# Kernel optimization log

Hardware: AMD Instinct MI355X
Metric: run time of the kernel (lower is better)

## Reference

```python
import jax, jax.numpy as jnp
import numpy as np


def _elu(x):
    return jnp.where(x > 0, x, jnp.expm1(x))


def setup_inputs() -> dict:
    key = jax.random.key(0)
    ks = jax.random.split(key, 12)
    B, T, E, A, S, H, L = 1024, 50, 1024, 6, 200, 200, 30
    g = lambda k, shape, s=0.05: (jax.random.normal(k, shape, jnp.float32) * s)
    return {
        "action": jax.random.normal(ks[0], (B, T, A), jnp.float32),
        "embed": jax.random.normal(ks[1], (B, T, E), jnp.float32),
        "noise": jax.random.normal(ks[2], (B, T, L), jnp.float32),
        # GRUCell params (PyTorch gate order r,z,n), stored as [in, 3S]
        "W_ih": g(ks[3], (A + E, 3 * S)),
        "W_hh": g(ks[4], (S, 3 * S)),
        "b_ih": jnp.zeros((3 * S,), jnp.float32),
        "b_hh": jnp.zeros((3 * S,), jnp.float32),
        # fc_prior: Linear(S,H) -> ELU -> Linear(H, 2L)
        "Wp1": g(ks[5], (S, H)), "bp1": jnp.zeros((H,), jnp.float32),
        "Wp2": g(ks[6], (H, 2 * L)), "bp2": jnp.zeros((2 * L,), jnp.float32),
        # fc_posterior: Linear(S+E,H) -> ELU -> Linear(H, 2L)
        "Wq1": g(ks[7], (S + E, H)), "bq1": jnp.zeros((H,), jnp.float32),
        "Wq2": g(ks[8], (H, 2 * L)), "bq2": jnp.zeros((2 * L,), jnp.float32),
    }


def reference(action, embed, noise, W_ih, W_hh, b_ih, b_hh,
              Wp1, bp1, Wp2, bp2, Wq1, bq1, Wq2, bq2):
    B = action.shape[0]
    S = W_hh.shape[0]

    def gru(x, h):
        # PyTorch GRUCell: gates r, z, n
        gi = x @ W_ih + b_ih
        gh = h @ W_hh + b_hh
        i_r, i_z, i_n = jnp.split(gi, 3, -1)
        h_r, h_z, h_n = jnp.split(gh, 3, -1)
        r = jax.nn.sigmoid(i_r + h_r)
        z = jax.nn.sigmoid(i_z + h_z)
        n = jnp.tanh(i_n + r * h_n)
        return (1.0 - z) * n + z * h

    def step(deter, inp):
        a_t, e_t, eps_t = inp  # [B,A], [B,E], [B,L]
        deter = gru(jnp.concatenate([a_t, e_t], -1), deter)
        pm, ps = jnp.split(_elu(deter @ Wp1 + bp1) @ Wp2 + bp2, 2, -1)
        qm, qs = jnp.split(
            _elu(jnp.concatenate([deter, e_t], -1) @ Wq1 + bq1) @ Wq2 + bq2, 2, -1)
        ps = jax.nn.softplus(ps) + 0.1
        qs = jax.nn.softplus(qs) + 0.1
        stoch = qm + qs * eps_t  # posterior rsample
        return deter, (deter, stoch, pm, ps, qm, qs)

    deter0 = jnp.zeros((B, S), action.dtype)
    xs = (jnp.swapaxes(action, 0, 1),
          jnp.swapaxes(embed, 0, 1),
          jnp.swapaxes(noise, 0, 1))
    _, outs = jax.lax.scan(step, deter0, xs)
    # [T,B,*] -> [B,T,*]; pack (deter, stoch, prior mean/std, post mean/std)
    outs = [jnp.swapaxes(o, 0, 1) for o in outs]
    return jnp.concatenate(outs, -1)  # [B, T, S + 5L]
```

## Files before the change

### kernel.cpp

```cpp
#include <hip/hip_runtime.h>
#include <hip/hip_bf16.h>
#include <cstdint>


typedef __attribute__((ext_vector_type(8))) short   short8;
typedef __attribute__((ext_vector_type(8))) __bf16  bf16x8;
typedef __attribute__((ext_vector_type(4))) float   f32x4;

__device__ __forceinline__ float bf2f(unsigned short u) {
    unsigned int v = ((unsigned int)u) << 16;
    return __builtin_bit_cast(float, v);
}
__device__ __forceinline__ unsigned short f2bf(float f) {
    unsigned int v = __builtin_bit_cast(unsigned int, f);
    v = v + 0x7FFFu + ((v >> 16) & 1u);
    return (unsigned short)(v >> 16);
}
__device__ __forceinline__ float softplusf(float x) {
    return (x > 20.f) ? x : log1pf(__expf(x));
}
__device__ __forceinline__ void gload_lds16(const void* g, void* l) {
    __builtin_amdgcn_global_load_lds(
        (const __attribute__((address_space(1))) void*)g,
        (__attribute__((address_space(3))) void*)l, 16, 0, 0);
}

#define OFF_BPACK 81920000
#define OFF_WHH   83558400
#define OFF_WPQ1  83837952
#define OFF_WPQ2  84024320


__global__ __launch_bounds__(256) void pack_kernel(
    const float* __restrict__ W_ih, const float* __restrict__ W_hh,
    const float* __restrict__ Wp1,  const float* __restrict__ Wq1,
    const float* __restrict__ Wp2,  const float* __restrict__ Wq2,
    unsigned short* __restrict__ Bpack, unsigned short* __restrict__ Whh_p,
    unsigned short* __restrict__ Wpq1,  unsigned short* __restrict__ Wpq2)
{
    int e = blockIdx.x * 256 + threadIdx.x;
    if (e < 819200) {
        const int j = e & 7, l = (e >> 3) & 63;
        const int nt = (e >> 9) % 50, kk = e / (512 * 50);
        const int k = kk * 32 + (l >> 4) * 8 + j;
        const int c = nt * 16 + (l & 15);
        Bpack[e] = f2bf((c < 600) ? W_ih[(6 + k) * 600 + c]
                                  : Wq1[(200 + k) * 200 + (c - 600)]);
        return;
    }
    e -= 819200;
    if (e < 139776) {
        const int j = e & 7, l = (e >> 3) & 63;
        const int nt = (e >> 9) % 39, kk = e / (512 * 39);
        const int k = kk * 32 + (l >> 4) * 8 + j;
        const int g = nt / 13, st = nt % 13;
        const int c = st * 16 + (l & 15);
        Whh_p[e] = (k < 200 && c < 200) ? f2bf(W_hh[k * 600 + g * 200 + c]) : (unsigned short)0;
        return;
    }
    e -= 139776;
    if (e < 93184) {
        const int j = e & 7, l = (e >> 3) & 63;
        const int nt = (e >> 9) % 26, kk = e / (512 * 26);
        const int k = kk * 32 + (l >> 4) * 8 + j;
        unsigned short v = 0;
        if (nt < 13) { const int c = nt * 16 + (l & 15);        if (k < 200 && c < 200) v = f2bf(Wp1[k * 200 + c]); }
        else         { const int c = (nt - 13) * 16 + (l & 15); if (k < 200 && c < 200) v = f2bf(Wq1[k * 200 + c]); }
        Wpq1[e] = v;
        return;
    }
    e -= 93184;
    if (e < 28672) {
        const int j = e & 7, l = (e >> 3) & 63;
        const int nt = (e >> 9) % 8, kk = e / (512 * 8);
        const int k = kk * 32 + (l >> 4) * 8 + j;
        unsigned short v = 0;
        if (nt < 4) { const int c = nt * 16 + (l & 15);       if (k < 200 && c < 60) v = f2bf(Wp2[k * 60 + c]); }
        else        { const int c = (nt - 4) * 16 + (l & 15); if (k < 200 && c < 60) v = f2bf(Wq2[k * 60 + c]); }
        Wpq2[e] = v;
    }
}

__global__ __launch_bounds__(512, 4) void k1_gi(
    const float* __restrict__ embed,
    const float* __restrict__ action,
    const float* __restrict__ W_ih,
    const float* __restrict__ b_ih,
    const float* __restrict__ bq1,
    const unsigned short* __restrict__ Bpack,
    unsigned short* __restrict__ GI)
{
    __shared__ unsigned short Bb[2][12800];
    __shared__ unsigned short Ab[2][2048];

    const int tid = threadIdx.x;
    const int w = tid >> 6, l = tid & 63;
    const int lo = l & 15, hi = l >> 4;
    const int mp = w >> 1, nq = w & 1;
    const int mblk = blockIdx.x >> 1;
    const int half = blockIdx.x & 1;
    const int tb = nq * 13;
    const int nn = nq ? 12 : 13;
    const int rb = mblk * 64;

    const unsigned short* Bsrc0 = Bpack + (size_t)half * 25 * 512;

    const int s = tid >> 1, j0 = (tid & 1) * 4;
    const int smp = s >> 6, sl = s & 63;
    const int srow = rb + smp * 16 + (sl & 15);
    const int sk = ((sl >> 4) * 8) + j0;
    const float* aSrc = embed + (size_t)srow * 1024 + sk;

    f32x4 acc[13];
#pragma unroll
    for (int i = 0; i < 13; ++i) acc[i] = f32x4{0.f, 0.f, 0.f, 0.f};

    {
#pragma unroll
        for (int i = 0; i < 4; ++i) {
            const int base = i * 512 + w * 64;
            if (base < 1600)
                gload_lds16(Bsrc0 + (size_t)(base + l) * 8, &Bb[0][base * 8]);
        }
        f32x4 a0 = *(const f32x4*)(aSrc);
        unsigned int w0 = (unsigned int)f2bf(a0[0]) | ((unsigned int)f2bf(a0[1]) << 16);
        unsigned int w1 = (unsigned int)f2bf(a0[2]) | ((unsigned int)f2bf(a0[3]) << 16);
        *(unsigned int*)&Ab[0][tid * 4]     = w0;
        *(unsigned int*)&Ab[0][tid * 4 + 2] = w1;
    }
    __syncthreads();

    int cur = 0;
    for (int kk = 0; kk < 32; ++kk) {
        const int nxt = cur ^ 1;
        const bool pf = (kk < 31);
        f32x4 an = f32x4{0.f, 0.f, 0.f, 0.f};
        if (pf) {
            const unsigned short* bs = Bsrc0 + (size_t)(kk + 1) * 50 * 512;
#pragma unroll
            for (int i = 0; i < 4; ++i) {
                const int base = i * 512 + w * 64;
                if (base < 1600)
                    gload_lds16(bs + (size_t)(base + l) * 8, &Bb[nxt][base * 8]);
            }
            an = *(const f32x4*)(aSrc + (size_t)(kk + 1) * 32);
        }

        bf16x8 af = __builtin_bit_cast(bf16x8, *(const short8*)&Ab[cur][(mp * 64 + l) * 8]);
#pragma unroll
        for (int i = 0; i < 13; ++i) if (i < nn) {
            bf16x8 b = __builtin_bit_cast(bf16x8, *(const short8*)&Bb[cur][(tb + i) * 512 + l * 8]);
            acc[i] = __builtin_amdgcn_mfma_f32_16x16x32_bf16(af, b, acc[i], 0, 0, 0);
        }

        if (pf) {
            unsigned int w0 = (unsigned int)f2bf(an[0]) | ((unsigned int)f2bf(an[1]) << 16);
            unsigned int w1 = (unsigned int)f2bf(an[2]) | ((unsigned int)f2bf(an[3]) << 16);
            *(unsigned int*)&Ab[nxt][tid * 4]     = w0;
            *(unsigned int*)&Ab[nxt][tid * 4 + 2] = w1;
        }
        __syncthreads();
        cur = nxt;
    }

    const int rbase = rb + mp * 16 + hi * 4;
    float av[4][6];
#pragma unroll
    for (int r = 0; r < 4; ++r)
#pragma unroll
        for (int k = 0; k < 6; ++k) av[r][k] = action[(size_t)(rbase + r) * 6 + k];
#pragma unroll
    for (int i = 0; i < 13; ++i) if (i < nn) {
        const int col = (half * 25 + tb + i) * 16 + lo;
        const float bias = (col < 600) ? b_ih[col] : bq1[col - 600];
        float wa[6];
        if (col < 600) {
#pragma unroll
            for (int k = 0; k < 6; ++k) wa[k] = W_ih[k * 600 + col];
        }
#pragma unroll
        for (int r = 0; r < 4; ++r) {
            float v = acc[i][r] + bias;
            if (col < 600) {
#pragma unroll
                for (int k = 0; k < 6; ++k) v += av[r][k] * wa[k];
            }
            GI[(size_t)(rbase + r) * 800 + col] = f2bf(v);
        }
    }
}

#define HSTRB 232
#define GSTR  227

__global__ __launch_bounds__(512, 2) void k2_scan(
    unsigned short* __restrict__ GI,
    const unsigned short* __restrict__ Whh_p,
    const float* __restrict__ b_hh,
    float* __restrict__ out)
{
    __shared__ unsigned short hS[16 * HSTRB];
    __shared__ float gAll[3 * 16 * GSTR];
    __shared__ __align__(16) unsigned short GIbuf[2][12288];

    const int tid = threadIdx.x;
    const int w = tid >> 6, l = tid & 63;
    const int lo = l & 15, hi = l >> 4;
    const int r0 = blockIdx.x * 16;

    for (int i = tid; i < 16 * HSTRB; i += 512) hS[i] = 0;

    const int t0 = w * 5;
    const int ntl = (w == 7) ? 4 : 5;
    bf16x8 wf[5][7];
#pragma unroll
    for (int i = 0; i < 5; ++i)
#pragma unroll
        for (int kk = 0; kk < 7; ++kk)
            if (i < ntl)
                wf[i][kk] = __builtin_bit_cast(bf16x8,
                    *(const short8*)&Whh_p[((kk * 39 + (t0 + i)) * 64 + l) * 8]);

    int gOff[5];
#pragma unroll
    for (int i = 0; i < 5; ++i) {
        int nt = t0 + i; if (nt > 38) nt = 38;
        const int g = nt / 13, st = nt - g * 13;
        gOff[i] = (g * 16 + hi * 4) * GSTR + st * 16 + lo;
    }

    const char* srcB[3];
#pragma unroll
    for (int i = 0; i < 3; ++i) {
        int j = (i * 8 + w) * 64 + l;
        int rj = j / 75; int cj = j - rj * 75;
        if (rj > 15) { rj = 15; cj = 74; }
        srcB[i] = (const char*)GI + (size_t)(r0 + rj) * 50 * 1600 + (size_t)cj * 16;
    }

    const int c = tid & 255;
    const int rh = tid >> 8;
    const bool act = (c < 200);
    float bh0 = 0.f, bh1 = 0.f, bh2 = 0.f;
    if (act) { bh0 = b_hh[c]; bh1 = b_hh[200 + c]; bh2 = b_hh[400 + c]; }
    float h_reg[8] = {0.f, 0.f, 0.f, 0.f, 0.f, 0.f, 0.f, 0.f};

    {
#pragma unroll
        for (int i = 0; i < 3; ++i)
            gload_lds16(srcB[i], &GIbuf[0][(i * 8 + w) * 512]);
    }
    asm volatile("s_waitcnt lgkmcnt(0)" ::: "memory");
    __builtin_amdgcn_s_barrier();
    __builtin_amdgcn_sched_barrier(0);

    for (int t = 0; t < 50; ++t) {
        const int tn = (t < 49) ? t + 1 : 49;
        const int bsel = (t + 1) & 1;
#pragma unroll
        for (int i = 0; i < 3; ++i)
            gload_lds16(srcB[i] + (size_t)tn * 1600, &GIbuf[bsel][(i * 8 + w) * 512]);

        bf16x8 hf[7];
#pragma unroll
        for (int kk = 0; kk < 7; ++kk)
            hf[kk] = __builtin_bit_cast(bf16x8,
                *(const short8*)&hS[lo * HSTRB + kk * 32 + hi * 8]);
        f32x4 acc[5];
#pragma unroll
        for (int i = 0; i < 5; ++i) acc[i] = f32x4{0.f, 0.f, 0.f, 0.f};
#pragma unroll
        for (int i = 0; i < 5; ++i) if (i < ntl)
#pragma unroll
            for (int kk = 0; kk < 7; ++kk)
                acc[i] = __builtin_amdgcn_mfma_f32_16x16x32_bf16(hf[kk], wf[i][kk], acc[i], 0, 0, 0);

#pragma unroll
        for (int i = 0; i < 5; ++i) if (i < ntl)
#pragma unroll
            for (int r = 0; r < 4; ++r)
                gAll[gOff[i] + r * GSTR] = acc[i][r];

        asm volatile("s_waitcnt lgkmcnt(0)" ::: "memory");
        __builtin_amdgcn_s_barrier();
        __builtin_amdgcn_sched_barrier(0);
        asm volatile("s_waitcnt vmcnt(3)" ::: "memory");
        __builtin_amdgcn_sched_barrier(0);

        if (act) {
            const unsigned short* gib = &GIbuf[t & 1][0];
#pragma unroll
            for (int rr = 0; rr < 8; ++rr) {
                const int row = rh * 8 + rr;
                const float gi_r = bf2f(gib[row * 600 + c]);
                const float gi_z = bf2f(gib[row * 600 + 200 + c]);
                const float gi_n = bf2f(gib[row * 600 + 400 + c]);
                const float gr = gi_r + gAll[(0 * 16 + row) * GSTR + c] + bh0;
                const float gz = gi_z + gAll[(1 * 16 + row) * GSTR + c] + bh1;
                const float hn = gAll[(2 * 16 + row) * GSTR + c] + bh2;
                const float rs = __builtin_amdgcn_rcpf(1.f + __expf(-gr));
                const float zz = __builtin_amdgcn_rcpf(1.f + __expf(-gz));
                const float x  = gi_n + rs * hn;
                const float e2 = __expf(-2.f * fabsf(x));
                float th = (1.f - e2) * __builtin_amdgcn_rcpf(1.f + e2);
                th = __builtin_copysignf(th, x);
                const float h = (1.f - zz) * th + zz * h_reg[rr];
                h_reg[rr] = h;
                hS[row * HSTRB + c] = f2bf(h);
                const size_t bt = (size_t)((r0 + row) * 50 + t);
                out[bt * 350 + c] = h;
                GI[bt * 800 + c]  = f2bf(h);
            }
        }

        asm volatile("s_waitcnt lgkmcnt(0)" ::: "memory");
        __builtin_amdgcn_s_barrier();
        __builtin_amdgcn_sched_barrier(0);
    }
}

__global__ __launch_bounds__(256, 1) void k3_heads(
    const unsigned short* __restrict__ GI,
    const unsigned short* __restrict__ Wpq1,
    const unsigned short* __restrict__ Wpq2,
    const float* __restrict__ noise,
    const float* __restrict__ bp1,
    const float* __restrict__ bp2,
    const float* __restrict__ bq2,
    float* __restrict__ out)
{
    __shared__ unsigned short pq[2][16 * HSTRB];
    __shared__ float ost[16 * 128];

    const int tid = threadIdx.x;
    const int w = tid >> 6, l = tid & 63;
    const int lo = l & 15, hi = l >> 4;
    const int r0 = blockIdx.x * 16;

    {   unsigned short* p0 = &pq[0][0];
        for (int i = tid; i < 2 * 16 * HSTRB; i += 256) p0[i] = 0; }
    __syncthreads();

    bf16x8 af[7];
#pragma unroll
    for (int kk = 0; kk < 7; ++kk)
        af[kk] = __builtin_bit_cast(bf16x8,
            *(const short8*)&GI[(size_t)(r0 + lo) * 800 + kk * 32 + hi * 8]);

    const int h1s = (w < 2) ? 7 * w : 14 + 6 * (w - 2);
    const int h1n = (w < 2) ? 7 : 6;
    f32x4 a2[7];
#pragma unroll
    for (int i = 0; i < 7; ++i) a2[i] = f32x4{0.f, 0.f, 0.f, 0.f};
#pragma unroll
    for (int i = 0; i < 7; ++i) if (i < h1n) {
        const int nt = h1s + i;
#pragma unroll
        for (int kk = 0; kk < 7; ++kk) {
            bf16x8 b = __builtin_bit_cast(bf16x8,
                *(const short8*)&Wpq1[((kk * 26 + nt) * 64 + l) * 8]);
            a2[i] = __builtin_amdgcn_mfma_f32_16x16x32_bf16(af[kk], b, a2[i], 0, 0, 0);
        }
    }
#pragma unroll
    for (int i = 0; i < 7; ++i) if (i < h1n) {
        const int nt = h1s + i;
        const bool isq = (nt >= 13);
        const int c1 = (isq ? (nt - 13) : nt) * 16 + lo;
        if (c1 < 200) {
#pragma unroll
            for (int r = 0; r < 4; ++r) {
                const int row = hi * 4 + r;
                float v = a2[i][r];
                if (isq) v += bf2f(GI[(size_t)(r0 + row) * 800 + 600 + c1]);
                else     v += bp1[c1];
                v = (v > 0.f) ? v : expm1f(v);
                pq[isq ? 1 : 0][row * HSTRB + c1] = f2bf(v);
            }
        }
    }
    __syncthreads();

    const unsigned short* srcS = &pq[(w >= 2) ? 1 : 0][0];
    bf16x8 pf[7];
#pragma unroll
    for (int kk = 0; kk < 7; ++kk)
        pf[kk] = __builtin_bit_cast(bf16x8,
            *(const short8*)&srcS[lo * HSTRB + kk * 32 + hi * 8]);
    f32x4 a3[2];
    a3[0] = f32x4{0.f, 0.f, 0.f, 0.f};
    a3[1] = f32x4{0.f, 0.f, 0.f, 0.f};
#pragma unroll
    for (int i = 0; i < 2; ++i) {
        const int nt = ((w >= 2) ? 4 : 0) + (w & 1) * 2 + i;
#pragma unroll
        for (int kk = 0; kk < 7; ++kk) {
            bf16x8 b = __builtin_bit_cast(bf16x8,
                *(const short8*)&Wpq2[((kk * 8 + nt) * 64 + l) * 8]);
            a3[i] = __builtin_amdgcn_mfma_f32_16x16x32_bf16(pf[kk], b, a3[i], 0, 0, 0);
        }
    }
#pragma unroll
    for (int i = 0; i < 2; ++i) {
        const int nt = ((w >= 2) ? 4 : 0) + (w & 1) * 2 + i;
        const int cl = (nt & 3) * 16 + lo;
        if (cl < 60) {
            const float bb = (nt < 4) ? bp2[cl] : bq2[cl];
            const int obase = ((nt < 4) ? 0 : 64) + ((cl < 30) ? cl : (32 + cl - 30));
#pragma unroll
            for (int r = 0; r < 4; ++r)
                ost[(hi * 4 + r) * 128 + obase] = a3[i][r] + bb;
        }
    }
    __syncthreads();

    for (int idx = tid; idx < 16 * 150; idx += 256) {
        const int row = idx / 150;
        const int c = 200 + (idx - row * 150);
        const size_t bt = (size_t)(r0 + row);
        const float* o = &ost[row * 128];
        float v;
        if (c < 230) {
            const int j = c - 200;
            const float qs = softplusf(o[96 + j]) + 0.1f;
            v = o[64 + j] + qs * noise[bt * 30 + j];
        }
        else if (c < 260) v = o[c - 230];
        else if (c < 290) v = softplusf(o[32 + (c - 260)]) + 0.1f;
        else if (c < 320) v = o[64 + (c - 290)];
        else              v = softplusf(o[96 + (c - 320)]) + 0.1f;
        out[bt * 350 + c] = v;
    }
}

extern "C" void kernel_launch(void* const* d_in, const int* in_sizes, int n_in,
                              void* d_out, int out_size, void* d_ws, size_t ws_size,
                              hipStream_t stream)
{
    const float* action = (const float*)d_in[0];
    const float* embed  = (const float*)d_in[1];
    const float* noise  = (const float*)d_in[2];
    const float* W_ih   = (const float*)d_in[3];
    const float* W_hh   = (const float*)d_in[4];
    const float* b_ih   = (const float*)d_in[5];
    const float* b_hh   = (const float*)d_in[6];
    const float* Wp1    = (const float*)d_in[7];
    const float* bp1    = (const float*)d_in[8];
    const float* Wp2    = (const float*)d_in[9];
    const float* bp2    = (const float*)d_in[10];
    const float* Wq1    = (const float*)d_in[11];
    const float* bq1    = (const float*)d_in[12];
    const float* Wq2    = (const float*)d_in[13];
    const float* bq2    = (const float*)d_in[14];
    (void)in_sizes; (void)n_in; (void)out_size; (void)ws_size;

    char* ws = (char*)d_ws;
    unsigned short* GI    = (unsigned short*)(ws);
    unsigned short* Bpack = (unsigned short*)(ws + OFF_BPACK);
    unsigned short* Whh_p = (unsigned short*)(ws + OFF_WHH);
    unsigned short* Wpq1  = (unsigned short*)(ws + OFF_WPQ1);
    unsigned short* Wpq2  = (unsigned short*)(ws + OFF_WPQ2);
    float* outp = (float*)d_out;

    pack_kernel<<<4222, 256, 0, stream>>>(W_ih, W_hh, Wp1, Wq1, Wp2, Wq2,
                                          Bpack, Whh_p, Wpq1, Wpq2);
    k1_gi<<<1600, 512, 0, stream>>>(embed, action, W_ih, b_ih, bq1, Bpack, GI);
    k2_scan<<<64, 512, 0, stream>>>(GI, Whh_p, b_hh, outp);
    k3_heads<<<3200, 256, 0, stream>>>(GI, Wpq1, Wpq2, noise, bp1, bp2, bq2, outp);
}
```

Measured before the change: 447.4 us.

## Retile input-projection GEMM to 128x160 tiles with async fp32 A staging

Restructures the k1 input-projection GEMM. Each 256-thread block now computes a 128-row by 160-column tile, with each wave doing 2x10 MFMAs so every B fragment is reused across two M subtiles. The fp32 embed tile is loaded straight into LDS with async global-to-LDS loads, alongside the packed weights, and converted to bf16 when the fragments are read. This replaces the register load, convert and LDS store path. Block indices are also swizzled so that blocks sharing a row block are spread across groups of eight. The aim is less LDS traffic per MFMA and fewer synchronous loads, at the cost of more LDS per block, more accumulator registers and per-iteration conversion work.

```diff
diff --git a/kernel.cpp b/kernel.cpp
--- a/kernel.cpp
+++ b/kernel.cpp
@@ -81,7 +81,8 @@
     }
 }
 
-__global__ __launch_bounds__(512, 4) void k1_gi(
+#define K1_BUF 13312
+__global__ __launch_bounds__(256, 3) void k1_gi(
     const float* __restrict__ embed,
     const float* __restrict__ action,
     const float* __restrict__ W_ih,
@@ -90,102 +91,108 @@
     const unsigned short* __restrict__ Bpack,
     unsigned short* __restrict__ GI)
 {
-    __shared__ unsigned short Bb[2][12800];
-    __shared__ unsigned short Ab[2][2048];
+    __shared__ short bufS[2][K1_BUF];
 
     const int tid = threadIdx.x;
     const int w = tid >> 6, l = tid & 63;
     const int lo = l & 15, hi = l >> 4;
-    const int mp = w >> 1, nq = w & 1;
-    const int mblk = blockIdx.x >> 1;
-    const int half = blockIdx.x & 1;
-    const int tb = nq * 13;
-    const int nn = nq ? 12 : 13;
-    const int rb = mblk * 64;
-
-    const unsigned short* Bsrc0 = Bpack + (size_t)half * 25 * 512;
-
-    const int s = tid >> 1, j0 = (tid & 1) * 4;
-    const int smp = s >> 6, sl = s & 63;
-    const int srow = rb + smp * 16 + (sl & 15);
-    const int sk = ((sl >> 4) * 8) + j0;
-    const float* aSrc = embed + (size_t)srow * 1024 + sk;
-
-    f32x4 acc[13];
-#pragma unroll
-    for (int i = 0; i < 13; ++i) acc[i] = f32x4{0.f, 0.f, 0.f, 0.f};
-
-    {
-#pragma unroll
-        for (int i = 0; i < 4; ++i) {
-            const int base = i * 512 + w * 64;
-            if (base < 1600)
-                gload_lds16(Bsrc0 + (size_t)(base + l) * 8, &Bb[0][base * 8]);
-        }
-        f32x4 a0 = *(const f32x4*)(aSrc);
-        unsigned int w0 = (unsigned int)f2bf(a0[0]) | ((unsigned int)f2bf(a0[1]) << 16);
-        unsigned int w1 = (unsigned int)f2bf(a0[2]) | ((unsigned int)f2bf(a0[3]) << 16);
-        *(unsigned int*)&Ab[0][tid * 4]     = w0;
-        *(unsigned int*)&Ab[0][tid * 4 + 2] = w1;
+
+    const int g    = (blockIdx.x & 7) * 250 + (blockIdx.x >> 3);
+    const int mblk = g / 5;
+    const int ng   = g - mblk * 5;
+    const int rb   = mblk * 128;
+
+    const char* sp[7]; int st[7]; int dof[7]; bool en[7];
+#pragma unroll
+    for (int i = 0; i < 7; ++i) {
+        const int j = w + 4 * i;
+        en[i] = (j < 26);
+        const int jc = (j < 26) ? j : 25;
+        if (jc < 10) {
+            sp[i]  = (const char*)(Bpack + (size_t)(ng * 10 + jc) * 512 + l * 8);
+            st[i]  = 50 * 512 * 2;
+            dof[i] = jc * 512;
+        } else {
+            const int a = jc - 10, m = a >> 1, h = a & 1;
+            sp[i]  = (const char*)(embed + (size_t)(rb + m * 16 + (l & 15)) * 1024
+                                         + (l >> 4) * 8 + h * 4);
+            st[i]  = 32 * 4;
+            dof[i] = 5120 + a * 512;
+        }
+    }
+
+    f32x4 acc[2][10];
+#pragma unroll
+    for (int m = 0; m < 2; ++m)
+#pragma unroll
+        for (int i = 0; i < 10; ++i) acc[m][i] = f32x4{0.f, 0.f, 0.f, 0.f};
+
+#pragma unroll
+    for (int i = 0; i < 7; ++i) if (en[i]) {
+        gload_lds16(sp[i], &bufS[0][dof[i]]);
+        sp[i] += st[i];
     }
     __syncthreads();
 
     int cur = 0;
     for (int kk = 0; kk < 32; ++kk) {
         const int nxt = cur ^ 1;
-        const bool pf = (kk < 31);
-        f32x4 an = f32x4{0.f, 0.f, 0.f, 0.f};
-        if (pf) {
-            const unsigned short* bs = Bsrc0 + (size_t)(kk + 1) * 50 * 512;
-#pragma unroll
-            for (int i = 0; i < 4; ++i) {
-                const int base = i * 512 + w * 64;
-                if (base < 1600)
-                    gload_lds16(bs + (size_t)(base + l) * 8, &Bb[nxt][base * 8]);
+        if (kk < 31) {
+#pragma unroll
+            for (int i = 0; i < 7; ++i) if (en[i]) {
+                gload_lds16(sp[i], &bufS[nxt][dof[i]]);
+                sp[i] += st[i];
             }
-            an = *(const f32x4*)(aSrc + (size_t)(kk + 1) * 32);
-        }
-
-        bf16x8 af = __builtin_bit_cast(bf16x8, *(const short8*)&Ab[cur][(mp * 64 + l) * 8]);
-#pragma unroll
-        for (int i = 0; i < 13; ++i) if (i < nn) {
-            bf16x8 b = __builtin_bit_cast(bf16x8, *(const short8*)&Bb[cur][(tb + i) * 512 + l * 8]);
-            acc[i] = __builtin_amdgcn_mfma_f32_16x16x32_bf16(af, b, acc[i], 0, 0, 0);
-        }
-
-        if (pf) {
-            unsigned int w0 = (unsigned int)f2bf(an[0]) | ((unsigned int)f2bf(an[1]) << 16);
-            unsigned int w1 = (unsigned int)f2bf(an[2]) | ((unsigned int)f2bf(an[3]) << 16);
-            *(unsigned int*)&Ab[nxt][tid * 4]     = w0;
-            *(unsigned int*)&Ab[nxt][tid * 4 + 2] = w1;
+        }
+
+        const float* Af = (const float*)&bufS[cur][5120];
+        bf16x8 af[2];
+#pragma unroll
+        for (int m = 0; m < 2; ++m) {
+            const int ms = w * 2 + m;
+            f32x4 v0 = *(const f32x4*)&Af[(ms * 2 + 0) * 256 + l * 4];
+            f32x4 v1 = *(const f32x4*)&Af[(ms * 2 + 1) * 256 + l * 4];
+            bf16x8 t;
+#pragma unroll
+            for (int q = 0; q < 4; ++q) { t[q] = (__bf16)v0[q]; t[4 + q] = (__bf16)v1[q]; }
+            af[m] = t;
+        }
+#pragma unroll
+        for (int i = 0; i < 10; ++i) {
+            bf16x8 b = __builtin_bit_cast(bf16x8, *(const short8*)&bufS[cur][i * 512 + l * 8]);
+            acc[0][i] = __builtin_amdgcn_mfma_f32_16x16x32_bf16(af[0], b, acc[0][i], 0, 0, 0);
+            acc[1][i] = __builtin_amdgcn_mfma_f32_16x16x32_bf16(af[1], b, acc[1][i], 0, 0, 0);
         }
         __syncthreads();
         cur = nxt;
     }
 
-    const int rbase = rb + mp * 16 + hi * 4;
-    float av[4][6];
-#pragma unroll
-    for (int r = 0; r < 4; ++r)
-#pragma unroll
-        for (int k = 0; k < 6; ++k) av[r][k] = action[(size_t)(rbase + r) * 6 + k];
-#pragma unroll
-    for (int i = 0; i < 13; ++i) if (i < nn) {
-        const int col = (half * 25 + tb + i) * 16 + lo;
-        const float bias = (col < 600) ? b_ih[col] : bq1[col - 600];
-        float wa[6];
-        if (col < 600) {
-#pragma unroll
-            for (int k = 0; k < 6; ++k) wa[k] = W_ih[k * 600 + col];
-        }
-#pragma unroll
-        for (int r = 0; r < 4; ++r) {
-            float v = acc[i][r] + bias;
+#pragma unroll
+    for (int m = 0; m < 2; ++m) {
+        const int rbase = rb + (w * 2 + m) * 16 + hi * 4;
+        float av[4][6];
+#pragma unroll
+        for (int r = 0; r < 4; ++r)
+#pragma unroll
+            for (int k = 0; k < 6; ++k) av[r][k] = action[(size_t)(rbase + r) * 6 + k];
+#pragma unroll
+        for (int i = 0; i < 10; ++i) {
+            const int col = ng * 160 + i * 16 + lo;
+            const float bias = (col < 600) ? b_ih[col] : bq1[col - 600];
+            float wa[6];
             if (col < 600) {
 #pragma unroll
-                for (int k = 0; k < 6; ++k) v += av[r][k] * wa[k];
+                for (int k = 0; k < 6; ++k) wa[k] = W_ih[k * 600 + col];
             }
-            GI[(size_t)(rbase + r) * 800 + col] = f2bf(v);
+#pragma unroll
+            for (int r = 0; r < 4; ++r) {
+                float v = acc[m][i][r] + bias;
+                if (col < 600) {
+#pragma unroll
+                    for (int k = 0; k < 6; ++k) v += av[r][k] * wa[k];
+                }
+                GI[(size_t)(rbase + r) * 800 + col] = f2bf(v);
+            }
         }
     }
 }
@@ -464,7 +471,7 @@
 
     pack_kernel<<<4222, 256, 0, stream>>>(W_ih, W_hh, Wp1, Wq1, Wp2, Wq2,
                                           Bpack, Whh_p, Wpq1, Wpq2);
-    k1_gi<<<1600, 512, 0, stream>>>(embed, action, W_ih, b_ih, bq1, Bpack, GI);
+    k1_gi<<<2000, 256, 0, stream>>>(embed, action, W_ih, b_ih, bq1, Bpack, GI);
     k2_scan<<<64, 512, 0, stream>>>(GI, Whh_p, b_hh, outp);
     k3_heads<<<3200, 256, 0, stream>>>(GI, Wpq1, Wpq2, noise, bp1, bp2, bq2, outp);
 }
```

Result: faster. 419.5 us (-6.2%).
